# Kernel tuning notes

Hardware: AMD Instinct MI355X
Metric: run time of the kernel (lower is better)

Reference implementation:

```python
import jax, jax.numpy as jnp
import numpy as np

D = 512        # model dim
H = 8          # num_heads (only used for the scale)
V = 32000      # output vocab
L = 3          # encoder / decoder stacks
SCALE = float((D // H) ** 0.5)


def _ln(x, g=None, b=None, eps=1e-5):
    m = jnp.mean(x, axis=-1, keepdims=True)
    v = jnp.var(x, axis=-1, keepdims=True)
    y = (x - m) * jax.lax.rsqrt(v + eps)
    if g is not None:
        y = y * g + b
    return y


def _attn(x, ctx, wq, wk, wv):
    # single-head attention (heads are never split in the original)
    q = x @ wq            # [B,S,D]
    k = ctx @ wk          # [B,T,D]
    v = ctx @ wv          # [B,T,D]
    s = jnp.einsum('bqd,bkd->bqk', q, k) / SCALE
    p = jax.nn.softmax(s, axis=-1)
    # residual + non-affine layer_norm (F.layer_norm with no weight/bias)
    return _ln(jnp.einsum('bqk,bkd->bqd', p, v) + x)


def setup_inputs() -> dict:
    key = jax.random.key(0)
    ks = jax.random.split(key, 20)
    w = lambda k, *s: jax.random.normal(k, s, jnp.float32) * 0.02
    return {
        'x': jax.random.normal(ks[0], (2, 2048, D), jnp.float32),
        'y': jax.random.normal(ks[1], (2, 2048, D), jnp.float32),
        'enc_wq': w(ks[2], L, D, D), 'enc_wk': w(ks[3], L, D, D), 'enc_wv': w(ks[4], L, D, D),
        'enc_fw': w(ks[5], L, D, D), 'enc_fb': jnp.zeros((L, D), jnp.float32),
        'enc_g': jnp.ones((L, D), jnp.float32), 'enc_b': jnp.zeros((L, D), jnp.float32),
        'dec_swq': w(ks[6], L, D, D), 'dec_swk': w(ks[7], L, D, D), 'dec_swv': w(ks[8], L, D, D),
        'dec_cwq': w(ks[9], L, D, D), 'dec_cwk': w(ks[10], L, D, D), 'dec_cwv': w(ks[11], L, D, D),
        'dec_fw': w(ks[12], L, D, D), 'dec_fb': jnp.zeros((L, D), jnp.float32),
        'dec_g': jnp.ones((L, D), jnp.float32), 'dec_b': jnp.zeros((L, D), jnp.float32),
        'fc_w': w(ks[13], D, V),
    }


def reference(x, y, enc_wq, enc_wk, enc_wv, enc_fw, enc_fb, enc_g, enc_b,
              dec_swq, dec_swk, dec_swv, dec_cwq, dec_cwk, dec_cwv,
              dec_fw, dec_fb, dec_g, dec_b, fc_w):
    # encoder stacks
    for i in range(L):
        x = _attn(x, x, enc_wq[i], enc_wk[i], enc_wv[i])
        x = _ln(jax.nn.silu(x @ enc_fw[i] + enc_fb[i]) + x, enc_g[i], enc_b[i])
    # decoder stacks: each receives (encoder_output, running decoder state)
    out = y
    for i in range(L):
        h = _attn(x, x, dec_swq[i], dec_swk[i], dec_swv[i])          # self-attn on encoder output
        h = _attn(h, out, dec_cwq[i], dec_cwk[i], dec_cwv[i])        # cross-attn: K,V from decoder state
        out = _ln(jax.nn.silu(h @ dec_fw[i] + dec_fb[i]) + h, dec_g[i], dec_b[i])
    return jax.nn.softmax(out @ fc_w, axis=-1)
```

## Files before the change

### kernel.cpp

```cpp
#include <hip/hip_runtime.h>
#include <math.h>

#define TDIM  512
#define NB    2
#define SLEN  2048
#define VOCAB 32000
#define NLAYER 3
#define NROW  (NB * SLEN)

typedef unsigned short u16;
typedef __attribute__((ext_vector_type(4))) float f32x4;
typedef __attribute__((ext_vector_type(8))) short bf16x8;

static const long SD  = (long)SLEN * TDIM;
static const long ST  = (long)SLEN * SLEN;
static const long ACT = (long)NB * SLEN * TDIM;
static const long DD  = (long)TDIM * TDIM;

__device__ __forceinline__ u16 f2bf(float x) {
    unsigned u = __builtin_bit_cast(unsigned, x);
    return (u16)((u + 0x7fffu + ((u >> 16) & 1u)) >> 16);
}
__device__ __forceinline__ float bf2f(u16 h) {
    unsigned u = ((unsigned)h) << 16;
    return __builtin_bit_cast(float, u);
}
__device__ __forceinline__ void split2(float v, u16& h, u16& l) {
    h = f2bf(v);
    l = f2bf(v - bf2f(h));
}

__device__ __forceinline__ void gl16(const u16* g, const u16* l) {
    __builtin_amdgcn_global_load_lds(
        (const __attribute__((address_space(1))) void*)g,
        (__attribute__((address_space(3))) void*)l, 16, 0, 0);
}

__device__ __forceinline__ float blockSum256(float v) {
    #pragma unroll
    for (int o = 32; o > 0; o >>= 1) v += __shfl_down(v, o);
    __shared__ float sm[4];
    __syncthreads();
    if ((threadIdx.x & 63) == 0) sm[threadIdx.x >> 6] = v;
    __syncthreads();
    return sm[0] + sm[1] + sm[2] + sm[3];
}

__device__ __forceinline__ float blockMax256(float v) {
    #pragma unroll
    for (int o = 32; o > 0; o >>= 1) v = fmaxf(v, __shfl_down(v, o));
    __shared__ float sm[4];
    __syncthreads();
    if ((threadIdx.x & 63) == 0) sm[threadIdx.x >> 6] = v;
    __syncthreads();
    return fmaxf(fmaxf(sm[0], sm[1]), fmaxf(sm[2], sm[3]));
}

template<int BM, int BN, bool SPLIT_OUT, bool BIAS>
__global__ __launch_bounds__(256)
void gemm_bf3(const u16* __restrict__ Ahi, const u16* __restrict__ Alo,
              const u16* __restrict__ Bhi, const u16* __restrict__ Blo,
              const float* __restrict__ bias,
              float* __restrict__ C, u16* __restrict__ Chi, u16* __restrict__ Clo,
              int K, int ldc, long sA, long sB, long sC, float alpha)
{
    constexpr int MI = BM / 32, NI = BN / 32;
    constexpr int IA = BM / 64, IB = BN / 64;
    __shared__ u16 lAh[BM][32], lAl[BM][32], lBh[BN][32], lBl[BN][32];
    Ahi += blockIdx.z * sA;  Alo += blockIdx.z * sA;
    Bhi += blockIdx.z * sB;  Blo += blockIdx.z * sB;
    const int bm = blockIdx.y * BM, bn = blockIdx.x * BN;
    const int tid = threadIdx.x;
    const int w = tid >> 6, l = tid & 63;
    const int wm = (w >> 1) * (BM / 2), wn = (w & 1) * (BN / 2);
    const int srow = l >> 2;
    const int skk  = (l & 3) * 8;
    const int frow = l & 15, fkk = (l >> 4) * 8;

    f32x4 acc[MI][NI] = {};

    for (int k0 = 0; k0 < K; k0 += 32) {
        #pragma unroll
        for (int i = 0; i < IA; ++i) {
            const int rr = (w * IA + i) * 16;
            const long go = (long)(bm + rr + srow) * K + k0 + skk;
            gl16(Ahi + go, &lAh[rr][0]);
            gl16(Alo + go, &lAl[rr][0]);
        }
        #pragma unroll
        for (int i = 0; i < IB; ++i) {
            const int rr = (w * IB + i) * 16;
            const long go = (long)(bn + rr + srow) * K + k0 + skk;
            gl16(Bhi + go, &lBh[rr][0]);
            gl16(Blo + go, &lBl[rr][0]);
        }
        __syncthreads();
        bf16x8 ah[MI], al[MI], bh[NI], bl[NI];
        #pragma unroll
        for (int m = 0; m < MI; ++m) {
            ah[m] = *(const bf16x8*)&lAh[wm + m * 16 + frow][fkk];
            al[m] = *(const bf16x8*)&lAl[wm + m * 16 + frow][fkk];
        }
        #pragma unroll
        for (int n = 0; n < NI; ++n) {
            bh[n] = *(const bf16x8*)&lBh[wn + n * 16 + frow][fkk];
            bl[n] = *(const bf16x8*)&lBl[wn + n * 16 + frow][fkk];
        }
        #pragma unroll
        for (int m = 0; m < MI; ++m)
            #pragma unroll
            for (int n = 0; n < NI; ++n) {
                acc[m][n] = __builtin_amdgcn_mfma_f32_16x16x32_bf16(al[m], bh[n], acc[m][n], 0, 0, 0);
                acc[m][n] = __builtin_amdgcn_mfma_f32_16x16x32_bf16(ah[m], bl[n], acc[m][n], 0, 0, 0);
                acc[m][n] = __builtin_amdgcn_mfma_f32_16x16x32_bf16(ah[m], bh[n], acc[m][n], 0, 0, 0);
            }
        __syncthreads();
    }

    if constexpr (SPLIT_OUT) { Chi += blockIdx.z * sC; Clo += blockIdx.z * sC; }
    else                     { C   += blockIdx.z * sC; }
    const int r0 = bm + wm + (l >> 4) * 4;
    const int c0 = bn + wn + (l & 15);
    #pragma unroll
    for (int m = 0; m < MI; ++m)
        #pragma unroll
        for (int n = 0; n < NI; ++n) {
            const int col = c0 + n * 16;
            float badd = 0.f;
            if constexpr (BIAS) badd = bias[col];
            #pragma unroll
            for (int r = 0; r < 4; ++r) {
                const long idx = (long)(r0 + m * 16 + r) * ldc + col;
                const float v = acc[m][n][r] * alpha + badd;
                if constexpr (SPLIT_OUT) {
                    u16 h, lo2; split2(v, h, lo2);
                    Chi[idx] = h; Clo[idx] = lo2;
                } else {
                    C[idx] = v;
                }
            }
        }
}

__global__ __launch_bounds__(256)
void split_rows(const float* __restrict__ in, u16* __restrict__ oh,
                u16* __restrict__ ol, long n4)
{
    long i = (long)blockIdx.x * 256 + threadIdx.x;
    if (i >= n4) return;
    float4 v = ((const float4*)in)[i];
    ushort4 h, l;
    split2(v.x, h.x, l.x); split2(v.y, h.y, l.y);
    split2(v.z, h.z, l.z); split2(v.w, h.w, l.w);
    ((ushort4*)oh)[i] = h; ((ushort4*)ol)[i] = l;
}

__global__ __launch_bounds__(256)
void transpose_split(const float* __restrict__ in, u16* __restrict__ oh,
                     u16* __restrict__ ol, int K, int N, long sIn, long sOut)
{
    __shared__ float t[32][33];
    in += (long)blockIdx.z * sIn;
    oh += (long)blockIdx.z * sOut;
    ol += (long)blockIdx.z * sOut;
    const int n0 = blockIdx.x * 32, k0 = blockIdx.y * 32;
    const int tx = threadIdx.x & 31, ty = threadIdx.x >> 5;
    #pragma unroll
    for (int r = 0; r < 4; ++r) {
        int k = ty * 4 + r;
        t[k][tx] = in[(long)(k0 + k) * N + n0 + tx];
    }
    __syncthreads();
    #pragma unroll
    for (int r = 0; r < 4; ++r) {
        int n = ty * 4 + r;
        float v = t[tx][n];
        u16 h, l2; split2(v, h, l2);
        long o = (long)(n0 + n) * K + k0 + tx;
        oh[o] = h; ol[o] = l2;
    }
}

__global__ __launch_bounds__(256)
void softmax2048(const float* __restrict__ s, u16* __restrict__ ph,
                 u16* __restrict__ pl)
{
    long row = blockIdx.x;
    const float* p = s + row * (long)SLEN;
    u16* oh = ph + row * (long)SLEN;
    u16* ol = pl + row * (long)SLEN;
    int t = threadIdx.x;
    float v[8], m = -INFINITY;
    #pragma unroll
    for (int i = 0; i < 8; ++i) { v[i] = p[t + 256 * i]; m = fmaxf(m, v[i]); }
    m = blockMax256(m);
    float sum = 0.f;
    #pragma unroll
    for (int i = 0; i < 8; ++i) { v[i] = expf(v[i] - m); sum += v[i]; }
    sum = blockSum256(sum);
    float inv = 1.0f / sum;
    #pragma unroll
    for (int i = 0; i < 8; ++i) {
        u16 h, l2; split2(v[i] * inv, h, l2);
        oh[t + 256 * i] = h; ol[t + 256 * i] = l2;
    }
}

__global__ __launch_bounds__(256)
void softmax_vocab(float* __restrict__ out)
{
    long row = blockIdx.x;
    float* p = out + row * (long)VOCAB;
    int t = threadIdx.x;
    float m = -INFINITY, s = 0.f;
    for (int i = t; i < VOCAB; i += 256) {
        float x = p[i];
        if (x > m) { s *= expf(m - x); m = x; }
        s += expf(x - m);
    }
    #pragma unroll
    for (int o = 32; o > 0; o >>= 1) {
        float m2 = __shfl_down(m, o), s2 = __shfl_down(s, o);
        float M = fmaxf(m, m2);
        s = s * expf(m - M) + s2 * expf(m2 - M);
        m = M;
    }
    __shared__ float sm[4], ss[4];
    if ((t & 63) == 0) { sm[t >> 6] = m; ss[t >> 6] = s; }
    __syncthreads();
    float M = fmaxf(fmaxf(sm[0], sm[1]), fmaxf(sm[2], sm[3]));
    float S = ss[0] * expf(sm[0] - M) + ss[1] * expf(sm[1] - M)
            + ss[2] * expf(sm[2] - M) + ss[3] * expf(sm[3] - M);
    float inv = 1.0f / S;
    for (int i = t; i < VOCAB; i += 256) p[i] = expf(p[i] - M) * inv;
}

template<int MODE>
__global__ __launch_bounds__(256)
void ln_row(const float* __restrict__ a, const float* __restrict__ r,
            const float* __restrict__ g, const float* __restrict__ b,
            float* __restrict__ y, u16* __restrict__ yh, u16* __restrict__ yl)
{
    long row = blockIdx.x;
    const float* pa = a + row * (long)TDIM;
    const float* pr = r + row * (long)TDIM;
    float* py = y + row * (long)TDIM;
    u16* ph = yh + row * (long)TDIM;
    u16* pl = yl + row * (long)TDIM;
    int t = threadIdx.x;
    float v0 = pa[t], v1 = pa[t + 256];
    if (MODE == 1) {
        v0 = v0 / (1.0f + expf(-v0));
        v1 = v1 / (1.0f + expf(-v1));
    }
    v0 += pr[t]; v1 += pr[t + 256];
    float mean = blockSum256(v0 + v1) * (1.0f / TDIM);
    float d0 = v0 - mean, d1 = v1 - mean;
    float var = blockSum256(d0 * d0 + d1 * d1) * (1.0f / TDIM);
    float inv = rsqrtf(var + 1e-5f);
    float y0 = d0 * inv, y1 = d1 * inv;
    if (MODE == 1) {
        y0 = y0 * g[t] + b[t];
        y1 = y1 * g[t + 256] + b[t + 256];
    }
    py[t] = y0; py[t + 256] = y1;
    u16 h0, l0, h1, l1;
    split2(y0, h0, l0); split2(y1, h1, l1);
    ph[t] = h0;       pl[t] = l0;
    ph[t + 256] = h1; pl[t + 256] = l1;
}

extern "C" void kernel_launch(void* const* d_in, const int* in_sizes, int n_in,
                              void* d_out, int out_size, void* d_ws, size_t ws_size,
                              hipStream_t stream)
{
    (void)in_sizes; (void)n_in; (void)out_size; (void)ws_size;
    const float* X   = (const float*)d_in[0];
    const float* Y   = (const float*)d_in[1];
    const float* EWQ = (const float*)d_in[2];
    const float* EWK = (const float*)d_in[3];
    const float* EWV = (const float*)d_in[4];
    const float* EFW = (const float*)d_in[5];
    const float* EFB = (const float*)d_in[6];
    const float* EG  = (const float*)d_in[7];
    const float* EB  = (const float*)d_in[8];
    const float* DSQ = (const float*)d_in[9];
    const float* DSK = (const float*)d_in[10];
    const float* DSV = (const float*)d_in[11];
    const float* DCQ = (const float*)d_in[12];
    const float* DCK = (const float*)d_in[13];
    const float* DCV = (const float*)d_in[14];
    const float* DFW = (const float*)d_in[15];
    const float* DFB = (const float*)d_in[16];
    const float* DG  = (const float*)d_in[17];
    const float* DB  = (const float*)d_in[18];
    const float* FCW = (const float*)d_in[19];
    float* OUT = (float*)d_out;

    char* p = (char*)d_ws;
    auto AF = [&](long n) { float* r = (float*)p; p += n * 4; return r; };
    auto AH = [&](long n) { u16*   r = (u16*)p;   p += n * 2; return r; };
    float* bx  = AF(ACT);
    float* bt  = AF(ACT);
    float* bv  = AF(ACT);
    float* bh1 = AF(ACT);
    float* bh2 = AF(ACT);
    float* bo  = AF(ACT);
    float* bs  = AF((long)NB * ST);
    u16 *xs_h = AH(ACT), *xs_l = AH(ACT);
    u16 *h1_h = AH(ACT), *h1_l = AH(ACT);
    u16 *h2_h = AH(ACT), *h2_l = AH(ACT);
    u16 *os_h = AH(ACT), *os_l = AH(ACT);
    u16 *qs_h = AH(ACT), *qs_l = AH(ACT);
    u16 *ks_h = AH(ACT), *ks_l = AH(ACT);
    u16 *vt_h = AH(ACT), *vt_l = AH(ACT);
    u16 *ps_h = AH((long)NB * ST), *ps_l = AH((long)NB * ST);
    u16 *W_h[11], *W_l[11];
    for (int i = 0; i < 11; ++i) { W_h[i] = AH(3 * DD); W_l[i] = AH(3 * DD); }
    u16 *fc_h = AH((long)TDIM * VOCAB), *fc_l = AH((long)TDIM * VOCAB);

    dim3 blk(256);

    hipMemcpyAsync(bx, X, ACT * 4, hipMemcpyDeviceToDevice, stream);
    hipMemcpyAsync(bo, Y, ACT * 4, hipMemcpyDeviceToDevice, stream);
    split_rows<<<dim3(ACT / 1024), blk, 0, stream>>>(X, xs_h, xs_l, ACT / 4);
    split_rows<<<dim3(ACT / 1024), blk, 0, stream>>>(Y, os_h, os_l, ACT / 4);
    const float* Wsrc[11] = {EWQ, EWK, EWV, EFW, DSQ, DSK, DSV, DCQ, DCK, DCV, DFW};
    for (int i = 0; i < 11; ++i)
        transpose_split<<<dim3(16, 16, 3), blk, 0, stream>>>(
            Wsrc[i], W_h[i], W_l[i], TDIM, TDIM, DD, DD);
    transpose_split<<<dim3(VOCAB / 32, 16, 1), blk, 0, stream>>>(
        FCW, fc_h, fc_l, TDIM, VOCAB, 0, 0);

    auto attn = [&](const float* xqf, const u16* xqh, const u16* xql,
                    const u16* cxh, const u16* cxl,
                    const u16* wqh, const u16* wql, const u16* wkh, const u16* wkl,
                    const u16* wvh, const u16* wvl,
                    float* dst, u16* dsth, u16* dstl) {
        gemm_bf3<64, 128, true, false><<<dim3(TDIM / 128, NROW / 64, 1), blk, 0, stream>>>(
            xqh, xql, wqh, wql, nullptr, nullptr, qs_h, qs_l, TDIM, TDIM, 0, 0, 0, 1.0f);
        gemm_bf3<64, 128, true, false><<<dim3(TDIM / 128, NROW / 64, 1), blk, 0, stream>>>(
            cxh, cxl, wkh, wkl, nullptr, nullptr, ks_h, ks_l, TDIM, TDIM, 0, 0, 0, 1.0f);
        gemm_bf3<64, 128, false, false><<<dim3(TDIM / 128, NROW / 64, 1), blk, 0, stream>>>(
            cxh, cxl, wvh, wvl, nullptr, bv, nullptr, nullptr, TDIM, TDIM, 0, 0, 0, 1.0f);
        transpose_split<<<dim3(TDIM / 32, SLEN / 32, NB), blk, 0, stream>>>(
            bv, vt_h, vt_l, SLEN, TDIM, SD, SD);
        gemm_bf3<128, 128, false, false><<<dim3(SLEN / 128, SLEN / 128, NB), blk, 0, stream>>>(
            qs_h, qs_l, ks_h, ks_l, nullptr, bs, nullptr, nullptr, TDIM, SLEN, SD, SD, ST, 0.125f);
        softmax2048<<<dim3(NROW), blk, 0, stream>>>(bs, ps_h, ps_l);
        gemm_bf3<64, 128, false, false><<<dim3(TDIM / 128, SLEN / 64, NB), blk, 0, stream>>>(
            ps_h, ps_l, vt_h, vt_l, nullptr, bt, nullptr, nullptr, SLEN, TDIM, ST, SD, SD, 1.0f);
        ln_row<0><<<dim3(NROW), blk, 0, stream>>>(bt, xqf, nullptr, nullptr, dst, dsth, dstl);
    };
    auto ffn = [&](const float* xf, const u16* xh, const u16* xl,
                   const u16* fwh, const u16* fwl, const float* fb,
                   const float* g_, const float* b_,
                   float* dst, u16* dh, u16* dl) {
        gemm_bf3<64, 128, false, true><<<dim3(TDIM / 128, NROW / 64, 1), blk, 0, stream>>>(
            xh, xl, fwh, fwl, fb, bt, nullptr, nullptr, TDIM, TDIM, 0, 0, 0, 1.0f);
        ln_row<1><<<dim3(NROW), blk, 0, stream>>>(bt, xf, g_, b_, dst, dh, dl);
    };

    for (int i = 0; i < NLAYER; ++i) {
        attn(bx, xs_h, xs_l, xs_h, xs_l,
             W_h[0] + i * DD, W_l[0] + i * DD, W_h[1] + i * DD, W_l[1] + i * DD,
             W_h[2] + i * DD, W_l[2] + i * DD, bx, xs_h, xs_l);
        ffn(bx, xs_h, xs_l, W_h[3] + i * DD, W_l[3] + i * DD,
            EFB + i * TDIM, EG + i * TDIM, EB + i * TDIM, bx, xs_h, xs_l);
    }

    for (int i = 0; i < NLAYER; ++i) {
        attn(bx, xs_h, xs_l, xs_h, xs_l,
             W_h[4] + i * DD, W_l[4] + i * DD, W_h[5] + i * DD, W_l[5] + i * DD,
             W_h[6] + i * DD, W_l[6] + i * DD, bh1, h1_h, h1_l);
        attn(bh1, h1_h, h1_l, os_h, os_l,
             W_h[7] + i * DD, W_l[7] + i * DD, W_h[8] + i * DD, W_l[8] + i * DD,
             W_h[9] + i * DD, W_l[9] + i * DD, bh2, h2_h, h2_l);
        ffn(bh2, h2_h, h2_l, W_h[10] + i * DD, W_l[10] + i * DD,
            DFB + i * TDIM, DG + i * TDIM, DB + i * TDIM, bo, os_h, os_l);
    }

    gemm_bf3<128, 128, false, false><<<dim3(VOCAB / 128, NROW / 128, 1), blk, 0, stream>>>(
        os_h, os_l, fc_h, fc_l, nullptr, OUT, nullptr, nullptr, TDIM, VOCAB, 0, 0, 0, 1.0f);
    softmax_vocab<<<dim3(NROW), blk, 0, stream>>>(OUT);
}
```

Baseline: 3.300 ms.

## Fuse Q/K projections, compute V transposed, widen GEMM K-tile with swizzled LDS

The GEMM kernel now stages 64-wide K tiles with an XOR-swizzled LDS layout to avoid bank conflicts, takes explicit leading dimensions, and can optionally remap workgroups for L2 locality (used by the vocab projection, now 64x128 tiles). Q and K weights are concatenated so self-attention computes both in one GEMM. V is produced directly in transposed split form as W^T·ctx^T, which drops the fp32 V buffer and the separate transpose kernel. Redundant initial device copies are removed. The cost is extra LDS per block and possibly lower occupancy.

```diff
diff --git a/kernel.cpp b/kernel.cpp
--- a/kernel.cpp
+++ b/kernel.cpp
@@ -16,6 +16,7 @@
 static const long ST  = (long)SLEN * SLEN;
 static const long ACT = (long)NB * SLEN * TDIM;
 static const long DD  = (long)TDIM * TDIM;
+static const long S2  = (long)SLEN * 1024;
 
 __device__ __forceinline__ u16 f2bf(float x) {
     unsigned u = __builtin_bit_cast(unsigned, x);
@@ -56,64 +57,79 @@
     return fmaxf(fmaxf(sm[0], sm[1]), fmaxf(sm[2], sm[3]));
 }
 
-template<int BM, int BN, bool SPLIT_OUT, bool BIAS>
-__global__ __launch_bounds__(256)
-void gemm_bf3(const u16* __restrict__ Ahi, const u16* __restrict__ Alo,
-              const u16* __restrict__ Bhi, const u16* __restrict__ Blo,
+template<int BM, int BN, bool SPLIT_OUT, bool BIAS, bool SWZ>
+__global__ __launch_bounds__(256)
+void gemm_bf3(const u16* __restrict__ Ahi, const u16* __restrict__ Alo, int lda,
+              const u16* __restrict__ Bhi, const u16* __restrict__ Blo, int ldb,
               const float* __restrict__ bias,
               float* __restrict__ C, u16* __restrict__ Chi, u16* __restrict__ Clo,
-              int K, int ldc, long sA, long sB, long sC, float alpha)
+              int ldc, int K, long sA, long sB, long sC, float alpha)
 {
     constexpr int MI = BM / 32, NI = BN / 32;
-    constexpr int IA = BM / 64, IB = BN / 64;
-    __shared__ u16 lAh[BM][32], lAl[BM][32], lBh[BN][32], lBl[BN][32];
+    constexpr int IA = BM / 32, IB = BN / 32;
+    __shared__ u16 lAh[BM][64], lAl[BM][64], lBh[BN][64], lBl[BN][64];
     Ahi += blockIdx.z * sA;  Alo += blockIdx.z * sA;
     Bhi += blockIdx.z * sB;  Blo += blockIdx.z * sB;
-    const int bm = blockIdx.y * BM, bn = blockIdx.x * BN;
+    int bxi = blockIdx.x, byi = blockIdx.y;
+    if (SWZ) {
+        const int nwg = gridDim.x * gridDim.y;
+        int bid = byi * gridDim.x + bxi;
+        bid = (bid & 7) * (nwg >> 3) + (bid >> 3);
+        bxi = bid % gridDim.x; byi = bid / gridDim.x;
+    }
+    const int bm = byi * BM, bn = bxi * BN;
     const int tid = threadIdx.x;
     const int w = tid >> 6, l = tid & 63;
     const int wm = (w >> 1) * (BM / 2), wn = (w & 1) * (BN / 2);
-    const int srow = l >> 2;
-    const int skk  = (l & 3) * 8;
-    const int frow = l & 15, fkk = (l >> 4) * 8;
+    const int srow = l >> 3;
+    const int scol = ((l & 7) ^ srow) * 8;
+    const int frow = l & 15, fk = (l >> 4) * 8;
+    const int rsw  = (frow & 7) * 8;
 
     f32x4 acc[MI][NI] = {};
 
-    for (int k0 = 0; k0 < K; k0 += 32) {
+    for (int k0 = 0; k0 < K; k0 += 64) {
         #pragma unroll
         for (int i = 0; i < IA; ++i) {
-            const int rr = (w * IA + i) * 16;
-            const long go = (long)(bm + rr + srow) * K + k0 + skk;
+            const int rr = (w * IA + i) * 8;
+            const long go = (long)(bm + rr + srow) * lda + k0 + scol;
             gl16(Ahi + go, &lAh[rr][0]);
             gl16(Alo + go, &lAl[rr][0]);
         }
         #pragma unroll
         for (int i = 0; i < IB; ++i) {
-            const int rr = (w * IB + i) * 16;
-            const long go = (long)(bn + rr + srow) * K + k0 + skk;
+            const int rr = (w * IB + i) * 8;
+            const long go = (long)(bn + rr + srow) * ldb + k0 + scol;
             gl16(Bhi + go, &lBh[rr][0]);
             gl16(Blo + go, &lBl[rr][0]);
         }
         __syncthreads();
-        bf16x8 ah[MI], al[MI], bh[NI], bl[NI];
         #pragma unroll
-        for (int m = 0; m < MI; ++m) {
-            ah[m] = *(const bf16x8*)&lAh[wm + m * 16 + frow][fkk];
-            al[m] = *(const bf16x8*)&lAl[wm + m * 16 + frow][fkk];
-        }
-        #pragma unroll
-        for (int n = 0; n < NI; ++n) {
-            bh[n] = *(const bf16x8*)&lBh[wn + n * 16 + frow][fkk];
-            bl[n] = *(const bf16x8*)&lBl[wn + n * 16 + frow][fkk];
-        }
-        #pragma unroll
-        for (int m = 0; m < MI; ++m)
+        for (int c = 0; c < 2; ++c) {
+            bf16x8 ah[MI], av[MI], bh[NI], bv[NI];
+            #pragma unroll
+            for (int m = 0; m < MI; ++m) {
+                const int row = wm + m * 16 + frow;
+                const int col = (c * 32 + fk) ^ rsw;
+                ah[m] = *(const bf16x8*)&lAh[row][col];
+                av[m] = *(const bf16x8*)&lAl[row][col];
+            }
             #pragma unroll
             for (int n = 0; n < NI; ++n) {
-                acc[m][n] = __builtin_amdgcn_mfma_f32_16x16x32_bf16(al[m], bh[n], acc[m][n], 0, 0, 0);
-                acc[m][n] = __builtin_amdgcn_mfma_f32_16x16x32_bf16(ah[m], bl[n], acc[m][n], 0, 0, 0);
-                acc[m][n] = __builtin_amdgcn_mfma_f32_16x16x32_bf16(ah[m], bh[n], acc[m][n], 0, 0, 0);
+                const int row = wn + n * 16 + frow;
+                const int col = (c * 32 + fk) ^ rsw;
+                bh[n] = *(const bf16x8*)&lBh[row][col];
+                bv[n] = *(const bf16x8*)&lBl[row][col];
             }
+            #pragma unroll
+            for (int m = 0; m < MI; ++m)
+                #pragma unroll
+                for (int n = 0; n < NI; ++n) {
+                    acc[m][n] = __builtin_amdgcn_mfma_f32_16x16x32_bf16(av[m], bh[n], acc[m][n], 0, 0, 0);
+                    acc[m][n] = __builtin_amdgcn_mfma_f32_16x16x32_bf16(ah[m], bv[n], acc[m][n], 0, 0, 0);
+                    acc[m][n] = __builtin_amdgcn_mfma_f32_16x16x32_bf16(ah[m], bh[n], acc[m][n], 0, 0, 0);
+                }
+        }
         __syncthreads();
     }
 
@@ -302,7 +318,6 @@
     auto AH = [&](long n) { u16*   r = (u16*)p;   p += n * 2; return r; };
     float* bx  = AF(ACT);
     float* bt  = AF(ACT);
-    float* bv  = AF(ACT);
     float* bh1 = AF(ACT);
     float* bh2 = AF(ACT);
     float* bo  = AF(ACT);
@@ -311,76 +326,104 @@
     u16 *h1_h = AH(ACT), *h1_l = AH(ACT);
     u16 *h2_h = AH(ACT), *h2_l = AH(ACT);
     u16 *os_h = AH(ACT), *os_l = AH(ACT);
-    u16 *qs_h = AH(ACT), *qs_l = AH(ACT);
-    u16 *ks_h = AH(ACT), *ks_l = AH(ACT);
+    u16 *qk_h = AH((long)NROW * 1024), *qk_l = AH((long)NROW * 1024);
     u16 *vt_h = AH(ACT), *vt_l = AH(ACT);
     u16 *ps_h = AH((long)NB * ST), *ps_l = AH((long)NB * ST);
-    u16 *W_h[11], *W_l[11];
-    for (int i = 0; i < 11; ++i) { W_h[i] = AH(3 * DD); W_l[i] = AH(3 * DD); }
-    u16 *fc_h = AH((long)TDIM * VOCAB), *fc_l = AH((long)TDIM * VOCAB);
+    u16 *eqk_h = AH(3 * 2 * DD), *eqk_l = AH(3 * 2 * DD);
+    u16 *ev_h  = AH(3 * DD),     *ev_l  = AH(3 * DD);
+    u16 *dsqk_h= AH(3 * 2 * DD), *dsqk_l= AH(3 * 2 * DD);
+    u16 *dsv_h = AH(3 * DD),     *dsv_l = AH(3 * DD);
+    u16 *dcqk_h= AH(3 * 2 * DD), *dcqk_l= AH(3 * 2 * DD);
+    u16 *dcv_h = AH(3 * DD),     *dcv_l = AH(3 * DD);
+    u16 *efw_h = AH(3 * DD),     *efw_l = AH(3 * DD);
+    u16 *dfw_h = AH(3 * DD),     *dfw_l = AH(3 * DD);
+    u16 *fc_h  = AH((long)TDIM * VOCAB), *fc_l = AH((long)TDIM * VOCAB);
 
     dim3 blk(256);
 
-    hipMemcpyAsync(bx, X, ACT * 4, hipMemcpyDeviceToDevice, stream);
-    hipMemcpyAsync(bo, Y, ACT * 4, hipMemcpyDeviceToDevice, stream);
     split_rows<<<dim3(ACT / 1024), blk, 0, stream>>>(X, xs_h, xs_l, ACT / 4);
     split_rows<<<dim3(ACT / 1024), blk, 0, stream>>>(Y, os_h, os_l, ACT / 4);
-    const float* Wsrc[11] = {EWQ, EWK, EWV, EFW, DSQ, DSK, DSV, DCQ, DCK, DCV, DFW};
-    for (int i = 0; i < 11; ++i)
-        transpose_split<<<dim3(16, 16, 3), blk, 0, stream>>>(
-            Wsrc[i], W_h[i], W_l[i], TDIM, TDIM, DD, DD);
-    transpose_split<<<dim3(VOCAB / 32, 16, 1), blk, 0, stream>>>(
-        FCW, fc_h, fc_l, TDIM, VOCAB, 0, 0);
-
-    auto attn = [&](const float* xqf, const u16* xqh, const u16* xql,
-                    const u16* cxh, const u16* cxl,
-                    const u16* wqh, const u16* wql, const u16* wkh, const u16* wkl,
-                    const u16* wvh, const u16* wvl,
-                    float* dst, u16* dsth, u16* dstl) {
-        gemm_bf3<64, 128, true, false><<<dim3(TDIM / 128, NROW / 64, 1), blk, 0, stream>>>(
-            xqh, xql, wqh, wql, nullptr, nullptr, qs_h, qs_l, TDIM, TDIM, 0, 0, 0, 1.0f);
-        gemm_bf3<64, 128, true, false><<<dim3(TDIM / 128, NROW / 64, 1), blk, 0, stream>>>(
-            cxh, cxl, wkh, wkl, nullptr, nullptr, ks_h, ks_l, TDIM, TDIM, 0, 0, 0, 1.0f);
-        gemm_bf3<64, 128, false, false><<<dim3(TDIM / 128, NROW / 64, 1), blk, 0, stream>>>(
-            cxh, cxl, wvh, wvl, nullptr, bv, nullptr, nullptr, TDIM, TDIM, 0, 0, 0, 1.0f);
-        transpose_split<<<dim3(TDIM / 32, SLEN / 32, NB), blk, 0, stream>>>(
-            bv, vt_h, vt_l, SLEN, TDIM, SD, SD);
-        gemm_bf3<128, 128, false, false><<<dim3(SLEN / 128, SLEN / 128, NB), blk, 0, stream>>>(
-            qs_h, qs_l, ks_h, ks_l, nullptr, bs, nullptr, nullptr, TDIM, SLEN, SD, SD, ST, 0.125f);
+    transpose_split<<<dim3(16, 16, 3), blk, 0, stream>>>(EWQ, eqk_h,      eqk_l,      TDIM, TDIM, DD, 2 * DD);
+    transpose_split<<<dim3(16, 16, 3), blk, 0, stream>>>(EWK, eqk_h + DD, eqk_l + DD, TDIM, TDIM, DD, 2 * DD);
+    transpose_split<<<dim3(16, 16, 3), blk, 0, stream>>>(EWV, ev_h,  ev_l,  TDIM, TDIM, DD, DD);
+    transpose_split<<<dim3(16, 16, 3), blk, 0, stream>>>(DSQ, dsqk_h,      dsqk_l,      TDIM, TDIM, DD, 2 * DD);
+    transpose_split<<<dim3(16, 16, 3), blk, 0, stream>>>(DSK, dsqk_h + DD, dsqk_l + DD, TDIM, TDIM, DD, 2 * DD);
+    transpose_split<<<dim3(16, 16, 3), blk, 0, stream>>>(DSV, dsv_h, dsv_l, TDIM, TDIM, DD, DD);
+    transpose_split<<<dim3(16, 16, 3), blk, 0, stream>>>(DCQ, dcqk_h,      dcqk_l,      TDIM, TDIM, DD, 2 * DD);
+    transpose_split<<<dim3(16, 16, 3), blk, 0, stream>>>(DCK, dcqk_h + DD, dcqk_l + DD, TDIM, TDIM, DD, 2 * DD);
+    transpose_split<<<dim3(16, 16, 3), blk, 0, stream>>>(DCV, dcv_h, dcv_l, TDIM, TDIM, DD, DD);
+    transpose_split<<<dim3(16, 16, 3), blk, 0, stream>>>(EFW, efw_h, efw_l, TDIM, TDIM, DD, DD);
+    transpose_split<<<dim3(16, 16, 3), blk, 0, stream>>>(DFW, dfw_h, dfw_l, TDIM, TDIM, DD, DD);
+    transpose_split<<<dim3(VOCAB / 32, 16, 1), blk, 0, stream>>>(FCW, fc_h, fc_l, TDIM, VOCAB, 0, 0);
+
+    auto attn_core = [&](const float* resf, const u16* ctxh, const u16* ctxl,
+                         const u16* vwh, const u16* vwl,
+                         float* dst, u16* dsth, u16* dstl) {
+        gemm_bf3<64, 128, true, false, false><<<dim3(16, 8, NB), blk, 0, stream>>>(
+            vwh, vwl, TDIM, ctxh, ctxl, TDIM, nullptr,
+            nullptr, vt_h, vt_l, SLEN, TDIM, 0, SD, SD, 1.0f);
+        gemm_bf3<64, 128, false, false, false><<<dim3(16, 32, NB), blk, 0, stream>>>(
+            qk_h, qk_l, 1024, qk_h + 512, qk_l + 512, 1024, nullptr,
+            bs, nullptr, nullptr, SLEN, TDIM, S2, S2, ST, 0.125f);
         softmax2048<<<dim3(NROW), blk, 0, stream>>>(bs, ps_h, ps_l);
-        gemm_bf3<64, 128, false, false><<<dim3(TDIM / 128, SLEN / 64, NB), blk, 0, stream>>>(
-            ps_h, ps_l, vt_h, vt_l, nullptr, bt, nullptr, nullptr, SLEN, TDIM, ST, SD, SD, 1.0f);
-        ln_row<0><<<dim3(NROW), blk, 0, stream>>>(bt, xqf, nullptr, nullptr, dst, dsth, dstl);
+        gemm_bf3<64, 128, false, false, false><<<dim3(4, 32, NB), blk, 0, stream>>>(
+            ps_h, ps_l, SLEN, vt_h, vt_l, SLEN, nullptr,
+            bt, nullptr, nullptr, TDIM, SLEN, ST, SD, SD, 1.0f);
+        ln_row<0><<<dim3(NROW), blk, 0, stream>>>(bt, resf, nullptr, nullptr, dst, dsth, dstl);
+    };
+    auto attn_self = [&](const float* xf, const u16* xh, const u16* xl,
+                         const u16* qkwh, const u16* qkwl,
+                         const u16* vwh, const u16* vwl,
+                         float* dst, u16* dsth, u16* dstl) {
+        gemm_bf3<64, 128, true, false, false><<<dim3(8, 64, 1), blk, 0, stream>>>(
+            xh, xl, TDIM, qkwh, qkwl, TDIM, nullptr,
+            nullptr, qk_h, qk_l, 1024, TDIM, 0, 0, 0, 1.0f);
+        attn_core(xf, xh, xl, vwh, vwl, dst, dsth, dstl);
+    };
+    auto attn_cross = [&](const float* qf, const u16* qh, const u16* ql,
+                          const u16* ch, const u16* cl,
+                          const u16* qkwh, const u16* qkwl,
+                          const u16* vwh, const u16* vwl,
+                          float* dst, u16* dsth, u16* dstl) {
+        gemm_bf3<64, 128, true, false, false><<<dim3(4, 64, 1), blk, 0, stream>>>(
+            qh, ql, TDIM, qkwh, qkwl, TDIM, nullptr,
+            nullptr, qk_h, qk_l, 1024, TDIM, 0, 0, 0, 1.0f);
+        gemm_bf3<64, 128, true, false, false><<<dim3(4, 64, 1), blk, 0, stream>>>(
+            ch, cl, TDIM, qkwh + DD, qkwl + DD, TDIM, nullptr,
+            nullptr, qk_h + 512, qk_l + 512, 1024, TDIM, 0, 0, 0, 1.0f);
+        attn_core(qf, ch, cl, vwh, vwl, dst, dsth, dstl);
     };
     auto ffn = [&](const float* xf, const u16* xh, const u16* xl,
                    const u16* fwh, const u16* fwl, const float* fb,
                    const float* g_, const float* b_,
                    float* dst, u16* dh, u16* dl) {
-        gemm_bf3<64, 128, false, true><<<dim3(TDIM / 128, NROW / 64, 1), blk, 0, stream>>>(
-            xh, xl, fwh, fwl, fb, bt, nullptr, nullptr, TDIM, TDIM, 0, 0, 0, 1.0f);
+        gemm_bf3<64, 128, false, true, false><<<dim3(4, 64, 1), blk, 0, stream>>>(
+            xh, xl, TDIM, fwh, fwl, TDIM, fb,
+            bt, nullptr, nullptr, TDIM, TDIM, 0, 0, 0, 1.0f);
         ln_row<1><<<dim3(NROW), blk, 0, stream>>>(bt, xf, g_, b_, dst, dh, dl);
     };
 
     for (int i = 0; i < NLAYER; ++i) {
-        attn(bx, xs_h, xs_l, xs_h, xs_l,
-             W_h[0] + i * DD, W_l[0] + i * DD, W_h[1] + i * DD, W_l[1] + i * DD,
-             W_h[2] + i * DD, W_l[2] + i * DD, bx, xs_h, xs_l);
-        ffn(bx, xs_h, xs_l, W_h[3] + i * DD, W_l[3] + i * DD,
+        attn_self(i == 0 ? X : bx, xs_h, xs_l,
+                  eqk_h + i * 2 * DD, eqk_l + i * 2 * DD,
+                  ev_h + i * DD, ev_l + i * DD, bx, xs_h, xs_l);
+        ffn(bx, xs_h, xs_l, efw_h + i * DD, efw_l + i * DD,
             EFB + i * TDIM, EG + i * TDIM, EB + i * TDIM, bx, xs_h, xs_l);
     }
 
     for (int i = 0; i < NLAYER; ++i) {
-        attn(bx, xs_h, xs_l, xs_h, xs_l,
-             W_h[4] + i * DD, W_l[4] + i * DD, W_h[5] + i * DD, W_l[5] + i * DD,
-             W_h[6] + i * DD, W_l[6] + i * DD, bh1, h1_h, h1_l);
-        attn(bh1, h1_h, h1_l, os_h, os_l,
-             W_h[7] + i * DD, W_l[7] + i * DD, W_h[8] + i * DD, W_l[8] + i * DD,
-             W_h[9] + i * DD, W_l[9] + i * DD, bh2, h2_h, h2_l);
-        ffn(bh2, h2_h, h2_l, W_h[10] + i * DD, W_l[10] + i * DD,
+        attn_self(bx, xs_h, xs_l,
+                  dsqk_h + i * 2 * DD, dsqk_l + i * 2 * DD,
+                  dsv_h + i * DD, dsv_l + i * DD, bh1, h1_h, h1_l);
+        attn_cross(bh1, h1_h, h1_l, os_h, os_l,
+                   dcqk_h + i * 2 * DD, dcqk_l + i * 2 * DD,
+                   dcv_h + i * DD, dcv_l + i * DD, bh2, h2_h, h2_l);
+        ffn(bh2, h2_h, h2_l, dfw_h + i * DD, dfw_l + i * DD,
             DFB + i * TDIM, DG + i * TDIM, DB + i * TDIM, bo, os_h, os_l);
     }
 
-    gemm_bf3<128, 128, false, false><<<dim3(VOCAB / 128, NROW / 128, 1), blk, 0, stream>>>(
-        os_h, os_l, fc_h, fc_l, nullptr, OUT, nullptr, nullptr, TDIM, VOCAB, 0, 0, 0, 1.0f);
+    gemm_bf3<64, 128, false, false, true><<<dim3(VOCAB / 128, NROW / 64, 1), blk, 0, stream>>>(
+        os_h, os_l, TDIM, fc_h, fc_l, TDIM, nullptr,
+        OUT, nullptr, nullptr, VOCAB, TDIM, 0, 0, 0, 1.0f);
     softmax_vocab<<<dim3(NROW), blk, 0, stream>>>(OUT);
 }
```

Result: faster. 3.057 ms (-7.3%).
